# Optimization experiments

Measured on AMD Instinct MI355X. Metric: run time of the kernel, lower is better.

Reference implementation:

```python
import jax, jax.numpy as jnp
import numpy as np

N = 100000
E = 3200000
HEADS = 4
DH = 16  # per-head dim
IN = 300
OUT2 = 32
SLOPE = 0.2  # PyG GATConv leaky_relu negative slope


def setup_inputs() -> dict:
    key = jax.random.key(0)
    ks = jax.random.split(key, 10)
    x = jax.random.normal(ks[0], (N, IN), dtype=jnp.float32)
    edge_index = jax.random.randint(ks[1], (2, E), 0, N, dtype=jnp.int64)
    sec_order_edge_index = jax.random.randint(ks[2], (2, E), 0, N, dtype=jnp.int64)
    # GATConv(300, 16, heads=4) params
    W1 = jax.random.normal(ks[3], (IN, HEADS * DH), dtype=jnp.float32) * (1.0 / np.sqrt(IN))
    att_src = jax.random.normal(ks[4], (HEADS, DH), dtype=jnp.float32) * 0.1
    att_dst = jax.random.normal(ks[5], (HEADS, DH), dtype=jnp.float32) * 0.1
    b1 = jnp.zeros((HEADS * DH,), dtype=jnp.float32)
    # GCNConv(64, 32) params
    W2 = jax.random.normal(ks[6], (HEADS * DH, OUT2), dtype=jnp.float32) * (1.0 / np.sqrt(HEADS * DH))
    b2 = jnp.zeros((OUT2,), dtype=jnp.float32)
    return {"x": x, "W1": W1, "att_src": att_src, "att_dst": att_dst, "b1": b1,
            "W2": W2, "b2": b2, "edge_index": edge_index,
            "sec_order_edge_index": sec_order_edge_index}


def _add_self_loops(edge_index, n):
    loop = jnp.arange(n, dtype=edge_index.dtype)
    src = jnp.concatenate([edge_index[0], loop])
    dst = jnp.concatenate([edge_index[1], loop])
    return src, dst


def _gat(x, W1, att_src, att_dst, b1, edge_index):
    n = x.shape[0]
    src, dst = _add_self_loops(edge_index, n)
    h = (x @ W1).reshape(n, HEADS, DH)                    # [N,H,D]
    a_s = jnp.einsum('nhd,hd->nh', h, att_src)            # [N,H]
    a_d = jnp.einsum('nhd,hd->nh', h, att_dst)
    e = jax.nn.leaky_relu(a_s[src] + a_d[dst], SLOPE)     # [Et,H]
    # segment softmax over edges grouped by destination node
    m = jax.ops.segment_max(e, dst, num_segments=n)       # [N,H]
    ex = jnp.exp(e - m[dst])
    denom = jax.ops.segment_sum(ex, dst, num_segments=n)  # [N,H] (>0: self-loops)
    alpha = ex / denom[dst]                               # [Et,H]
    out = jax.ops.segment_sum(h[src] * alpha[:, :, None], dst, num_segments=n)
    return out.reshape(n, HEADS * DH) + b1


def _gcn(x, W2, b2, edge_index):
    n = x.shape[0]
    src, dst = _add_self_loops(edge_index, n)
    deg = jax.ops.segment_sum(jnp.ones_like(dst, dtype=x.dtype), dst, num_segments=n)
    dinv = jnp.where(deg > 0, jax.lax.rsqrt(deg), 0.0)
    norm = dinv[src] * dinv[dst]                          # [Et]
    h = x @ W2                                            # [N,32]
    out = jax.ops.segment_sum(h[src] * norm[:, None], dst, num_segments=n)
    return out + b2


def reference(x, W1, att_src, att_dst, b1, W2, b2, edge_index, sec_order_edge_index):
    x1 = jax.nn.relu(_gat(x, W1, att_src, att_dst, b1, edge_index))
    # F.dropout with training=False is identity (eval mode)
    return _gcn(x1, W2, b2, sec_order_edge_index)
```

## Files before the change

kernel.cpp:

```cpp
#include <hip/hip_runtime.h>
#include <hip/hip_fp16.h>

#define N_NODES 100000
#define N_EDGES 3200000
#define TOT_E   (N_EDGES + N_NODES)
#define HEADS   4
#define DH      16
#define IN_F    300
#define HID     64
#define OUT2    32
#define SLOPE   0.2f
#define NBK     256
#define GSZ     391
#define EBLK    4096
#define NBA     ((TOT_E + EBLK - 1) / EBLK)

#define G1B_ROWS 64
#define G1B_KT   20
#define G1B_NT   15
#define G1B_XP   76

__global__ __launch_bounds__(64, 2) void k_gemm1(const float* __restrict__ x,
                                                 const float* __restrict__ W1,
                                                 __half* __restrict__ h16) {
    __shared__ __align__(16) float xT[G1B_KT][G1B_XP];
    __shared__ __align__(16) float wl[2][G1B_KT * HID];
    const int t = threadIdx.x;
    const int tc = t & 7, tr = t >> 3;
    const int c0 = tc * 8, r0 = tr * 8;
    const int row0 = blockIdx.x * G1B_ROWS;

    int rj[5], qj[5];
    const float* xp[5];
#pragma unroll
    for (int j = 0; j < 5; j++) {
        int c = j * 64 + t;
        int r = c / 5;
        rj[j] = r;
        qj[j] = c - r * 5;
        int gr = row0 + r;
        gr = (gr < N_NODES) ? gr : (N_NODES - 1);
        xp[j] = x + (size_t)gr * IN_F + qj[j] * 4;
    }

    float acc[8][8];
#pragma unroll
    for (int i = 0; i < 8; i++)
#pragma unroll
        for (int j = 0; j < 8; j++) acc[i][j] = 0.f;

    float4 xr[5];
#pragma unroll
    for (int j = 0; j < 5; j++) xr[j] = *(const float4*)(xp[j]);
#pragma unroll
    for (int m = 0; m < 5; m++)
        __builtin_amdgcn_global_load_lds(
            (const __attribute__((address_space(1))) unsigned int*)(W1 + m * 256 + t * 4),
            (__attribute__((address_space(3))) unsigned int*)(&wl[0][m * 256]),
            16, 0, 0);

    for (int tt = 0; tt < G1B_NT; ++tt) {
#pragma unroll
        for (int j = 0; j < 5; j++) {
            int r = rj[j], kq = qj[j] * 4;
            xT[kq + 0][r] = xr[j].x;
            xT[kq + 1][r] = xr[j].y;
            xT[kq + 2][r] = xr[j].z;
            xT[kq + 3][r] = xr[j].w;
        }
        asm volatile("s_waitcnt vmcnt(0)" ::: "memory");
        if (tt + 1 < G1B_NT) {
            const int kt = (tt + 1) * G1B_KT;
#pragma unroll
            for (int j = 0; j < 5; j++) xr[j] = *(const float4*)(xp[j] + kt);
            const float* wsrc = W1 + kt * HID;
            float* wdst = wl[(tt + 1) & 1];
#pragma unroll
            for (int m = 0; m < 5; m++)
                __builtin_amdgcn_global_load_lds(
                    (const __attribute__((address_space(1))) unsigned int*)(wsrc + m * 256 + t * 4),
                    (__attribute__((address_space(3))) unsigned int*)(wdst + m * 256),
                    16, 0, 0);
        }
        const float* wb = wl[tt & 1];
#pragma unroll 4
        for (int k = 0; k < G1B_KT; k++) {
            float4 xa = *(const float4*)&xT[k][r0];
            float4 xb = *(const float4*)&xT[k][r0 + 4];
            float4 wa = *(const float4*)&wb[k * HID + c0];
            float4 wc = *(const float4*)&wb[k * HID + c0 + 4];
            float xv[8] = {xa.x, xa.y, xa.z, xa.w, xb.x, xb.y, xb.z, xb.w};
            float wv[8] = {wa.x, wa.y, wa.z, wa.w, wc.x, wc.y, wc.z, wc.w};
#pragma unroll
            for (int i = 0; i < 8; i++)
#pragma unroll
                for (int j = 0; j < 8; j++)
                    acc[i][j] += xv[i] * wv[j];
        }
    }

#pragma unroll
    for (int i = 0; i < 8; i++) {
        int gr = row0 + r0 + i;
        if (gr < N_NODES) {
            __half2 q[4];
            q[0] = __floats2half2_rn(acc[i][0], acc[i][1]);
            q[1] = __floats2half2_rn(acc[i][2], acc[i][3]);
            q[2] = __floats2half2_rn(acc[i][4], acc[i][5]);
            q[3] = __floats2half2_rn(acc[i][6], acc[i][7]);
            *(float4*)&h16[(size_t)gr * HID + c0] = *(float4*)q;
        }
    }
}

__global__ void k_scores(const __half* __restrict__ h16,
                         const float* __restrict__ att_src,
                         const float* __restrict__ att_dst,
                         float* __restrict__ as_ad) {
    int tid = blockIdx.x * blockDim.x + threadIdx.x;
    if (tid >= N_NODES * HEADS) return;
    int n = tid >> 2, hd = tid & 3;
    const __half* hp = &h16[(size_t)n * HID + hd * DH];
    __half2 hv[8];
    *(float4*)&hv[0] = *(const float4*)hp;
    *(float4*)&hv[4] = *(const float4*)(hp + 8);
    float s = 0.f, d = 0.f;
#pragma unroll
    for (int k = 0; k < 8; k++) {
        float2 f = __half22float2(hv[k]);
        s += f.x * att_src[hd * DH + 2 * k] + f.y * att_src[hd * DH + 2 * k + 1];
        d += f.x * att_dst[hd * DH + 2 * k] + f.y * att_dst[hd * DH + 2 * k + 1];
    }
    as_ad[n * 8 + hd] = s;
    as_ad[n * 8 + 4 + hd] = d;
}

__global__ __launch_bounds__(512) void k_chist(const int* __restrict__ ei1,
                                               const int* __restrict__ ei2,
                                               int* __restrict__ ccnt) {
    __shared__ int hist[NBK];
    int b = blockIdx.x; const int* ei; int* cc;
    if (b < NBA) { ei = ei1; cc = ccnt; }
    else         { ei = ei2; cc = ccnt + NBK; b -= NBA; }
    int t = threadIdx.x;
    if (t < NBK) hist[t] = 0;
    __syncthreads();
    int e0 = b * EBLK;
#pragma unroll
    for (int i = 0; i < 8; i++) {
        int e = e0 + i * 512 + t;
        if (e < TOT_E) {
            int dst = (e < N_EDGES) ? ei[N_EDGES + e] : (e - N_EDGES);
            atomicAdd(&hist[(unsigned int)dst / GSZ], 1);
        }
    }
    __syncthreads();
    if (t < NBK) { int v = hist[t]; if (v) atomicAdd(&cc[t], v); }
}

__global__ __launch_bounds__(512) void k_cscan(const int* __restrict__ ccnt,
                                               int* __restrict__ crp,
                                               int* __restrict__ ccur) {
    __shared__ int sc[512];
    int t = threadIdx.x;
    int idx = t & (NBK - 1);
    int own = ccnt[t];
    sc[t] = own;
    __syncthreads();
    for (int off = 1; off < NBK; off <<= 1) {
        int v = (idx >= off) ? sc[t - off] : 0;
        __syncthreads();
        sc[t] += v;
        __syncthreads();
    }
    int ex = sc[t] - own;
    crp[t] = ex; ccur[t] = ex;
}

__global__ __launch_bounds__(512) void k_binA(const int* __restrict__ ei1,
                                              const int* __restrict__ ei2,
                                              int* __restrict__ ccur,
                                              unsigned int* __restrict__ tmp) {
    __shared__ int hist[NBK];
    __shared__ int base[NBK];
    int b = blockIdx.x; const int* ei; int loff;
    if (b < NBA) { ei = ei1; loff = 0; }
    else         { ei = ei2; loff = 1; b -= NBA; }
    int t = threadIdx.x;
    if (t < NBK) hist[t] = 0;
    __syncthreads();
    unsigned int pk[8]; int cb[8], rk[8];
    int e0 = b * EBLK;
#pragma unroll
    for (int i = 0; i < 8; i++) {
        int e = e0 + i * 512 + t;
        cb[i] = -1;
        if (e < TOT_E) {
            int src, dst;
            if (e < N_EDGES) { src = ei[e]; dst = ei[N_EDGES + e]; }
            else             { src = e - N_EDGES; dst = src; }
            unsigned int c   = (unsigned int)dst / GSZ;
            unsigned int dlo = (unsigned int)dst - c * GSZ;
            cb[i] = (int)c;
            pk[i] = (dlo << 17) | (unsigned int)src;
            rk[i] = atomicAdd(&hist[c], 1);
        }
    }
    __syncthreads();
    if (t < NBK) {
        int v = hist[t];
        base[t] = v ? atomicAdd(&ccur[loff * NBK + t], v) : 0;
    }
    __syncthreads();
    unsigned int* tp = tmp + (size_t)loff * TOT_E;
#pragma unroll
    for (int i = 0; i < 8; i++)
        if (cb[i] >= 0) tp[base[cb[i]] + rk[i]] = pk[i];
}

__global__ __launch_bounds__(256) void k_binB(const unsigned int* __restrict__ tmp,
                                              const int* __restrict__ crp,
                                              int* __restrict__ rowptr,
                                              int* __restrict__ srcs,
                                              float* __restrict__ dinv) {
    __shared__ int cnt[GSZ + 1];
    __shared__ int sc[512];
    __shared__ int cur[GSZ + 1];
    int blk = blockIdx.x;
    int l = blk >> 8, b = blk & 255;
    int t = threadIdx.x;
    int nbeg = b * GSZ;
    int ncnt = min(GSZ, N_NODES - nbeg);
    const int* crpl = crp + l * NBK;
    int ebeg = crpl[b];
    int eend = (b < NBK - 1) ? crpl[b + 1] : TOT_E;
    const unsigned int* tp = tmp + (size_t)l * TOT_E;
    for (int i = t; i < GSZ + 1; i += 256) cnt[i] = 0;
    __syncthreads();
    for (int e = ebeg + t; e < eend; e += 256)
        atomicAdd(&cnt[tp[e] >> 17], 1);
    __syncthreads();
    int t2 = t + 256;
    sc[t]  = (t  < ncnt) ? cnt[t]  : 0;
    sc[t2] = (t2 < ncnt) ? cnt[t2] : 0;
    __syncthreads();
    for (int off = 1; off < 512; off <<= 1) {
        int v0 = (t  >= off) ? sc[t  - off] : 0;
        int v1 = (t2 >= off) ? sc[t2 - off] : 0;
        __syncthreads();
        sc[t] += v0; sc[t2] += v1;
        __syncthreads();
    }
    for (int i = t; i < ncnt; i += 256) {
        int c = cnt[i];
        int gpos = ebeg + sc[i] - c;
        rowptr[l * N_NODES + nbeg + i] = gpos;
        cur[i] = gpos;
        if (l == 1) dinv[nbeg + i] = rsqrtf((float)c);
    }
    __syncthreads();
    int* so = srcs + (size_t)l * TOT_E;
    for (int e = ebeg + t; e < eend; e += 256) {
        unsigned int p = tp[e];
        int pos = atomicAdd(&cur[p >> 17], 1);
        so[pos] = (int)(p & 0x1FFFF);
    }
}

__global__ __launch_bounds__(256) void k_gat(const __half* __restrict__ h16,
                                             const float* __restrict__ as_ad,
                                             const int* __restrict__ rowptr,
                                             const int* __restrict__ srcs,
                                             const float* __restrict__ b1,
                                             float* __restrict__ x1) {
    int w = (blockIdx.x * 256 + threadIdx.x) >> 6;
    if (w >= N_NODES) return;
    int lane = threadIdx.x & 63;
    int eidx = lane >> 3;
    int cl = lane & 7;
    int hd = cl >> 1;
    int c0 = cl * 8;
    float ad = as_ad[w * 8 + 4 + hd];
    int beg = rowptr[w];
    int end = (w == N_NODES - 1) ? TOT_E : rowptr[w + 1];
    float l = 0.f;
    float a0 = 0.f, a1 = 0.f, a2 = 0.f, a3 = 0.f;
    float a4 = 0.f, a5 = 0.f, a6 = 0.f, a7 = 0.f;
#pragma unroll 2
    for (int j = beg; j < end; j += 8) {
        int je = j + eidx;
        int s = srcs[min(je, end - 1)];
        float4 raw = *(const float4*)&h16[(size_t)s * HID + c0];
        float e = as_ad[s * 8 + hd] + ad;
        e = fminf(fmaxf(e, SLOPE * e), 60.f);
        float p = (je < end) ? __expf(e) : 0.f;
        l += p;
        const __half2* hv = (const __half2*)&raw;
        float2 f0 = __half22float2(hv[0]);
        float2 f1 = __half22float2(hv[1]);
        float2 f2 = __half22float2(hv[2]);
        float2 f3 = __half22float2(hv[3]);
        a0 += p * f0.x; a1 += p * f0.y; a2 += p * f1.x; a3 += p * f1.y;
        a4 += p * f2.x; a5 += p * f2.y; a6 += p * f3.x; a7 += p * f3.y;
    }
    l  += __shfl_xor(l, 8, 64);  l  += __shfl_xor(l, 16, 64);  l  += __shfl_xor(l, 32, 64);
    a0 += __shfl_xor(a0, 8, 64); a0 += __shfl_xor(a0, 16, 64); a0 += __shfl_xor(a0, 32, 64);
    a1 += __shfl_xor(a1, 8, 64); a1 += __shfl_xor(a1, 16, 64); a1 += __shfl_xor(a1, 32, 64);
    a2 += __shfl_xor(a2, 8, 64); a2 += __shfl_xor(a2, 16, 64); a2 += __shfl_xor(a2, 32, 64);
    a3 += __shfl_xor(a3, 8, 64); a3 += __shfl_xor(a3, 16, 64); a3 += __shfl_xor(a3, 32, 64);
    a4 += __shfl_xor(a4, 8, 64); a4 += __shfl_xor(a4, 16, 64); a4 += __shfl_xor(a4, 32, 64);
    a5 += __shfl_xor(a5, 8, 64); a5 += __shfl_xor(a5, 16, 64); a5 += __shfl_xor(a5, 32, 64);
    a6 += __shfl_xor(a6, 8, 64); a6 += __shfl_xor(a6, 16, 64); a6 += __shfl_xor(a6, 32, 64);
    a7 += __shfl_xor(a7, 8, 64); a7 += __shfl_xor(a7, 16, 64); a7 += __shfl_xor(a7, 32, 64);
    if (eidx == 0) {
        float rl = 1.f / l;
        float4 b0 = *(const float4*)&b1[c0];
        float4 b4 = *(const float4*)&b1[c0 + 4];
        float4 o0 = make_float4(fmaxf(a0 * rl + b0.x, 0.f),
                                fmaxf(a1 * rl + b0.y, 0.f),
                                fmaxf(a2 * rl + b0.z, 0.f),
                                fmaxf(a3 * rl + b0.w, 0.f));
        float4 o4 = make_float4(fmaxf(a4 * rl + b4.x, 0.f),
                                fmaxf(a5 * rl + b4.y, 0.f),
                                fmaxf(a6 * rl + b4.z, 0.f),
                                fmaxf(a7 * rl + b4.w, 0.f));
        *(float4*)&x1[(size_t)w * HID + c0] = o0;
        *(float4*)&x1[(size_t)w * HID + c0 + 4] = o4;
    }
}

__global__ __launch_bounds__(256) void k_gemm2(const float* __restrict__ x1,
                                               const float* __restrict__ W2,
                                               const float* __restrict__ dinv,
                                               float* __restrict__ h2s) {
    __shared__ float wl[HID * OUT2];
    __shared__ float xl[8][HID];
    int t = threadIdx.x;
    for (int i = t; i < HID * OUT2; i += 256) wl[i] = W2[i];
    int row0 = blockIdx.x * 8;
    for (int i = t; i < 8 * HID; i += 256) {
        int rr = i >> 6, kk = i & 63;
        int gr = row0 + rr;
        xl[rr][kk] = (gr < N_NODES) ? x1[(size_t)gr * HID + kk] : 0.f;
    }
    __syncthreads();
    int r = t >> 5, c = t & 31;
    float acc = 0.f;
#pragma unroll 8
    for (int k = 0; k < HID; k++) acc += xl[r][k] * wl[k * OUT2 + c];
    int gr = row0 + r;
    if (gr < N_NODES) h2s[(size_t)gr * OUT2 + c] = acc * dinv[gr];
}

__global__ __launch_bounds__(256) void k_gcn(const float* __restrict__ h2s,
                                             const float* __restrict__ dinv,
                                             const int* __restrict__ rowptr,
                                             const int* __restrict__ srcs,
                                             const float* __restrict__ b2,
                                             float* __restrict__ out) {
    int w = (blockIdx.x * 256 + threadIdx.x) >> 6;
    if (w >= N_NODES) return;
    int lane = threadIdx.x & 63;
    int eidx = lane >> 3;
    int cq = lane & 7;
    int c0 = cq * 4;
    int beg = rowptr[w];
    int end = (w == N_NODES - 1) ? TOT_E : rowptr[w + 1];
    float ax = 0.f, ay = 0.f, az = 0.f, aw = 0.f;
#pragma unroll 2
    for (int j = beg; j < end; j += 8) {
        int je = j + eidx;
        int s = srcs[min(je, end - 1)];
        float4 h4 = *(const float4*)&h2s[(size_t)s * OUT2 + c0];
        if (je < end) { ax += h4.x; ay += h4.y; az += h4.z; aw += h4.w; }
    }
    ax += __shfl_xor(ax, 8, 64); ax += __shfl_xor(ax, 16, 64); ax += __shfl_xor(ax, 32, 64);
    ay += __shfl_xor(ay, 8, 64); ay += __shfl_xor(ay, 16, 64); ay += __shfl_xor(ay, 32, 64);
    az += __shfl_xor(az, 8, 64); az += __shfl_xor(az, 16, 64); az += __shfl_xor(az, 32, 64);
    aw += __shfl_xor(aw, 8, 64); aw += __shfl_xor(aw, 16, 64); aw += __shfl_xor(aw, 32, 64);
    if (eidx == 0) {
        float dv = dinv[w];
        float4 bv = *(const float4*)&b2[c0];
        float4 o = make_float4(ax * dv + bv.x, ay * dv + bv.y,
                               az * dv + bv.z, aw * dv + bv.w);
        *(float4*)&out[(size_t)w * OUT2 + c0] = o;
    }
}

static inline size_t align_up(size_t v, size_t a) { return (v + a - 1) & ~(a - 1); }

extern "C" void kernel_launch(void* const* d_in, const int* in_sizes, int n_in,
                              void* d_out, int out_size, void* d_ws, size_t ws_size,
                              hipStream_t stream) {
    const float* x       = (const float*)d_in[0];
    const float* W1      = (const float*)d_in[1];
    const float* att_src = (const float*)d_in[2];
    const float* att_dst = (const float*)d_in[3];
    const float* b1      = (const float*)d_in[4];
    const float* W2      = (const float*)d_in[5];
    const float* b2      = (const float*)d_in[6];
    const int*   ei1     = (const int*)d_in[7];
    const int*   ei2     = (const int*)d_in[8];
    float* out = (float*)d_out;

    char* p = (char*)d_ws;
    size_t off = 0;
    auto carve = [&](size_t bytes) { void* q = p + off; off = align_up(off + bytes, 256); return q; };
    __half* h16   = (__half*)carve((size_t)N_NODES * HID * 2);
    float* x1     = (float*)carve((size_t)N_NODES * HID * 4);
    float* h2s    = (float*)carve((size_t)N_NODES * OUT2 * 4);
    float* as_ad  = (float*)carve((size_t)N_NODES * 8 * 4);
    float* dinv   = (float*)carve((size_t)N_NODES * 4);
    int* rowptr   = (int*)carve((size_t)2 * N_NODES * 4);
    int* srcs     = (int*)carve((size_t)2 * TOT_E * 4);
    int* ccnt     = (int*)carve((size_t)2 * NBK * 4);
    int* crp      = (int*)carve((size_t)2 * NBK * 4);
    int* ccur     = (int*)carve((size_t)2 * NBK * 4);
    unsigned int* tmp = (unsigned int*)x1;
    (void)ws_size; (void)in_sizes; (void)n_in; (void)out_size;

    hipMemsetAsync(ccnt, 0, (size_t)2 * NBK * 4, stream);

    k_gemm1<<<(N_NODES + G1B_ROWS - 1) / G1B_ROWS, 64, 0, stream>>>(x, W1, h16);
    k_scores<<<(N_NODES * HEADS + 255) / 256, 256, 0, stream>>>(h16, att_src, att_dst, as_ad);

    k_chist<<<2 * NBA, 512, 0, stream>>>(ei1, ei2, ccnt);
    k_cscan<<<1, 512, 0, stream>>>(ccnt, crp, ccur);
    k_binA<<<2 * NBA, 512, 0, stream>>>(ei1, ei2, ccur, tmp);
    k_binB<<<2 * NBK, 256, 0, stream>>>(tmp, crp, rowptr, srcs, dinv);

    k_gat<<<N_NODES / 4, 256, 0, stream>>>(h16, as_ad, rowptr, srcs, b1, x1);

    k_gemm2<<<N_NODES / 8, 256, 0, stream>>>(x1, W2, dinv, h2s);

    k_gcn<<<N_NODES / 4, 256, 0, stream>>>(h2s, dinv, rowptr + N_NODES, srcs + TOT_E, b2, out);
}
```

Baseline: 572.2 us.

## Use fp16 MFMA for first GEMM and store GCN features in half precision

Replaces the scalar fp32 FMA GEMM for x@W1 with an MFMA 16x16x32 f16 kernel. x is converted to fp16 into swizzled LDS tiles, and a small pre-kernel writes W1 transposed and padded as fp16. Separately, the GCN pre-aggregation features h2s are stored as fp16, which halves the bytes read per edge in the gather, and the gcn kernel now handles 16 edges per iteration with 8 channels per lane. Both changes trade precision for lower compute and memory traffic, and add one extra small kernel launch.

```diff
diff --git a/kernel.cpp b/kernel.cpp
--- a/kernel.cpp
+++ b/kernel.cpp
@@ -15,100 +15,138 @@
 #define EBLK    4096
 #define NBA     ((TOT_E + EBLK - 1) / EBLK)
 
-#define G1B_ROWS 64
-#define G1B_KT   20
-#define G1B_NT   15
-#define G1B_XP   76
-
-__global__ __launch_bounds__(64, 2) void k_gemm1(const float* __restrict__ x,
-                                                 const float* __restrict__ W1,
-                                                 __half* __restrict__ h16) {
-    __shared__ __align__(16) float xT[G1B_KT][G1B_XP];
-    __shared__ __align__(16) float wl[2][G1B_KT * HID];
+typedef _Float16 f16x8 __attribute__((ext_vector_type(8)));
+typedef float    f32x4 __attribute__((ext_vector_type(4)));
+
+__global__ void k_wcvt(const float* __restrict__ W1, __half* __restrict__ BT16) {
+    int idx = blockIdx.x * 256 + threadIdx.x;
+    if (idx >= HID * 320) return;
+    int n = idx / 320, k = idx - n * 320;
+    BT16[idx] = (k < IN_F) ? __float2half(W1[(size_t)k * HID + n]) : __float2half(0.f);
+}
+
+#define G1_BM 128
+#define G1_BK 64
+#define G1_NS 5
+
+__global__ __launch_bounds__(256) void k_gemm1(const float* __restrict__ x,
+                                               const __half* __restrict__ BT16,
+                                               __half* __restrict__ h16) {
+    __shared__ _Float16 At[G1_BM][G1_BK];
+    __shared__ _Float16 Bt[HID][G1_BK];
     const int t = threadIdx.x;
-    const int tc = t & 7, tr = t >> 3;
-    const int c0 = tc * 8, r0 = tr * 8;
-    const int row0 = blockIdx.x * G1B_ROWS;
-
-    int rj[5], qj[5];
-    const float* xp[5];
-#pragma unroll
-    for (int j = 0; j < 5; j++) {
-        int c = j * 64 + t;
-        int r = c / 5;
-        rj[j] = r;
-        qj[j] = c - r * 5;
-        int gr = row0 + r;
+    const int lane = t & 63, w = t >> 6;
+    const int lr = lane & 15, lg = lane >> 4;
+    const int row0 = blockIdx.x * G1_BM;
+    const int wrow = w * 32;
+
+    int arow[4], auc[4];
+    const float* axp[4];
+#pragma unroll
+    for (int m = 0; m < 4; m++) {
+        int id = t + m * 256;
+        arow[m] = id >> 3; auc[m] = id & 7;
+        int gr = row0 + arow[m];
         gr = (gr < N_NODES) ? gr : (N_NODES - 1);
-        xp[j] = x + (size_t)gr * IN_F + qj[j] * 4;
-    }
-
-    float acc[8][8];
-#pragma unroll
-    for (int i = 0; i < 8; i++)
-#pragma unroll
-        for (int j = 0; j < 8; j++) acc[i][j] = 0.f;
-
-    float4 xr[5];
-#pragma unroll
-    for (int j = 0; j < 5; j++) xr[j] = *(const float4*)(xp[j]);
-#pragma unroll
-    for (int m = 0; m < 5; m++)
-        __builtin_amdgcn_global_load_lds(
-            (const __attribute__((address_space(1))) unsigned int*)(W1 + m * 256 + t * 4),
-            (__attribute__((address_space(3))) unsigned int*)(&wl[0][m * 256]),
-            16, 0, 0);
-
-    for (int tt = 0; tt < G1B_NT; ++tt) {
-#pragma unroll
-        for (int j = 0; j < 5; j++) {
-            int r = rj[j], kq = qj[j] * 4;
-            xT[kq + 0][r] = xr[j].x;
-            xT[kq + 1][r] = xr[j].y;
-            xT[kq + 2][r] = xr[j].z;
-            xT[kq + 3][r] = xr[j].w;
-        }
-        asm volatile("s_waitcnt vmcnt(0)" ::: "memory");
-        if (tt + 1 < G1B_NT) {
-            const int kt = (tt + 1) * G1B_KT;
-#pragma unroll
-            for (int j = 0; j < 5; j++) xr[j] = *(const float4*)(xp[j] + kt);
-            const float* wsrc = W1 + kt * HID;
-            float* wdst = wl[(tt + 1) & 1];
-#pragma unroll
-            for (int m = 0; m < 5; m++)
-                __builtin_amdgcn_global_load_lds(
-                    (const __attribute__((address_space(1))) unsigned int*)(wsrc + m * 256 + t * 4),
-                    (__attribute__((address_space(3))) unsigned int*)(wdst + m * 256),
-                    16, 0, 0);
-        }
-        const float* wb = wl[tt & 1];
-#pragma unroll 4
-        for (int k = 0; k < G1B_KT; k++) {
-            float4 xa = *(const float4*)&xT[k][r0];
-            float4 xb = *(const float4*)&xT[k][r0 + 4];
-            float4 wa = *(const float4*)&wb[k * HID + c0];
-            float4 wc = *(const float4*)&wb[k * HID + c0 + 4];
-            float xv[8] = {xa.x, xa.y, xa.z, xa.w, xb.x, xb.y, xb.z, xb.w};
-            float wv[8] = {wa.x, wa.y, wa.z, wa.w, wc.x, wc.y, wc.z, wc.w};
-#pragma unroll
-            for (int i = 0; i < 8; i++)
-#pragma unroll
-                for (int j = 0; j < 8; j++)
-                    acc[i][j] += xv[i] * wv[j];
-        }
-    }
-
-#pragma unroll
-    for (int i = 0; i < 8; i++) {
-        int gr = row0 + r0 + i;
-        if (gr < N_NODES) {
-            __half2 q[4];
-            q[0] = __floats2half2_rn(acc[i][0], acc[i][1]);
-            q[1] = __floats2half2_rn(acc[i][2], acc[i][3]);
-            q[2] = __floats2half2_rn(acc[i][4], acc[i][5]);
-            q[3] = __floats2half2_rn(acc[i][6], acc[i][7]);
-            *(float4*)&h16[(size_t)gr * HID + c0] = *(float4*)q;
+        axp[m] = x + (size_t)gr * IN_F + auc[m] * 8;
+    }
+    int bn[2], buc[2];
+    const __half* bxp[2];
+#pragma unroll
+    for (int q = 0; q < 2; q++) {
+        int id = t + q * 256;
+        bn[q] = id >> 3; buc[q] = id & 7;
+        bxp[q] = BT16 + bn[q] * (G1_BK * G1_NS) + buc[q] * 8;
+    }
+
+    float4 ar[4][2];
+    uint4  br[2];
+
+    auto loadS = [&](int kb) {
+        if (kb + G1_BK <= IN_F) {
+#pragma unroll
+            for (int m = 0; m < 4; m++) {
+                ar[m][0] = *(const float4*)(axp[m] + kb);
+                ar[m][1] = *(const float4*)(axp[m] + kb + 4);
+            }
+        } else {
+#pragma unroll
+            for (int m = 0; m < 4; m++) {
+                float v[8];
+#pragma unroll
+                for (int e = 0; e < 8; e++) {
+                    int k = kb + auc[m] * 8 + e;
+                    v[e] = (k < IN_F) ? axp[m][kb + e] : 0.f;
+                }
+                ar[m][0] = make_float4(v[0], v[1], v[2], v[3]);
+                ar[m][1] = make_float4(v[4], v[5], v[6], v[7]);
+            }
+        }
+#pragma unroll
+        for (int q = 0; q < 2; q++) br[q] = *(const uint4*)(bxp[q] + kb);
+    };
+
+    auto writeS = [&]() {
+#pragma unroll
+        for (int m = 0; m < 4; m++) {
+            f16x8 pk;
+            pk[0] = (_Float16)ar[m][0].x; pk[1] = (_Float16)ar[m][0].y;
+            pk[2] = (_Float16)ar[m][0].z; pk[3] = (_Float16)ar[m][0].w;
+            pk[4] = (_Float16)ar[m][1].x; pk[5] = (_Float16)ar[m][1].y;
+            pk[6] = (_Float16)ar[m][1].z; pk[7] = (_Float16)ar[m][1].w;
+            *(f16x8*)&At[arow[m]][(auc[m] ^ (arow[m] & 7)) << 3] = pk;
+        }
+#pragma unroll
+        for (int q = 0; q < 2; q++)
+            *(uint4*)&Bt[bn[q]][(buc[q] ^ (bn[q] & 7)) << 3] = br[q];
+    };
+
+    f32x4 acc[2][4];
+#pragma unroll
+    for (int mt = 0; mt < 2; mt++)
+#pragma unroll
+        for (int nt = 0; nt < 4; nt++) acc[mt][nt] = (f32x4){0.f, 0.f, 0.f, 0.f};
+
+    loadS(0);
+    for (int s = 0; s < G1_NS; s++) {
+        __syncthreads();
+        writeS();
+        if (s + 1 < G1_NS) loadS((s + 1) * G1_BK);
+        __syncthreads();
+#pragma unroll
+        for (int ks = 0; ks < 2; ks++) {
+            const int u = ks * 4 + lg;
+            f16x8 af[2], bf[4];
+#pragma unroll
+            for (int mt = 0; mt < 2; mt++) {
+                int r = wrow + mt * 16 + lr;
+                af[mt] = *(const f16x8*)&At[r][(u ^ (r & 7)) << 3];
+            }
+#pragma unroll
+            for (int nt = 0; nt < 4; nt++) {
+                int n = nt * 16 + lr;
+                bf[nt] = *(const f16x8*)&Bt[n][(u ^ (n & 7)) << 3];
+            }
+#pragma unroll
+            for (int mt = 0; mt < 2; mt++)
+#pragma unroll
+                for (int nt = 0; nt < 4; nt++)
+                    acc[mt][nt] = __builtin_amdgcn_mfma_f32_16x16x32_f16(
+                        af[mt], bf[nt], acc[mt][nt], 0, 0, 0);
+        }
+    }
+
+#pragma unroll
+    for (int mt = 0; mt < 2; mt++) {
+#pragma unroll
+        for (int rg = 0; rg < 4; rg++) {
+            int gr = row0 + wrow + mt * 16 + lg * 4 + rg;
+            if (gr < N_NODES) {
+#pragma unroll
+                for (int nt = 0; nt < 4; nt++)
+                    h16[(size_t)gr * HID + nt * 16 + lr] =
+                        __float2half((float)acc[mt][nt][rg]);
+            }
         }
     }
 }
@@ -332,7 +370,7 @@
 __global__ __launch_bounds__(256) void k_gemm2(const float* __restrict__ x1,
                                                const float* __restrict__ W2,
                                                const float* __restrict__ dinv,
-                                               float* __restrict__ h2s) {
+                                               __half* __restrict__ h2s) {
     __shared__ float wl[HID * OUT2];
     __shared__ float xl[8][HID];
     int t = threadIdx.x;
@@ -349,10 +387,10 @@
 #pragma unroll 8
     for (int k = 0; k < HID; k++) acc += xl[r][k] * wl[k * OUT2 + c];
     int gr = row0 + r;
-    if (gr < N_NODES) h2s[(size_t)gr * OUT2 + c] = acc * dinv[gr];
-}
-
-__global__ __launch_bounds__(256) void k_gcn(const float* __restrict__ h2s,
+    if (gr < N_NODES) h2s[(size_t)gr * OUT2 + c] = __float2half(acc * dinv[gr]);
+}
+
+__global__ __launch_bounds__(256) void k_gcn(const __half* __restrict__ h2s,
                                              const float* __restrict__ dinv,
                                              const int* __restrict__ rowptr,
                                              const int* __restrict__ srcs,
@@ -361,29 +399,46 @@
     int w = (blockIdx.x * 256 + threadIdx.x) >> 6;
     if (w >= N_NODES) return;
     int lane = threadIdx.x & 63;
-    int eidx = lane >> 3;
-    int cq = lane & 7;
-    int c0 = cq * 4;
+    int eidx = lane >> 2;
+    int cq = lane & 3;
+    int c0 = cq * 8;
     int beg = rowptr[w];
     int end = (w == N_NODES - 1) ? TOT_E : rowptr[w + 1];
-    float ax = 0.f, ay = 0.f, az = 0.f, aw = 0.f;
+    float a0 = 0.f, a1 = 0.f, a2 = 0.f, a3 = 0.f;
+    float a4 = 0.f, a5 = 0.f, a6 = 0.f, a7 = 0.f;
 #pragma unroll 2
-    for (int j = beg; j < end; j += 8) {
+    for (int j = beg; j < end; j += 16) {
         int je = j + eidx;
         int s = srcs[min(je, end - 1)];
-        float4 h4 = *(const float4*)&h2s[(size_t)s * OUT2 + c0];
-        if (je < end) { ax += h4.x; ay += h4.y; az += h4.z; aw += h4.w; }
-    }
-    ax += __shfl_xor(ax, 8, 64); ax += __shfl_xor(ax, 16, 64); ax += __shfl_xor(ax, 32, 64);
-    ay += __shfl_xor(ay, 8, 64); ay += __shfl_xor(ay, 16, 64); ay += __shfl_xor(ay, 32, 64);
-    az += __shfl_xor(az, 8, 64); az += __shfl_xor(az, 16, 64); az += __shfl_xor(az, 32, 64);
-    aw += __shfl_xor(aw, 8, 64); aw += __shfl_xor(aw, 16, 64); aw += __shfl_xor(aw, 32, 64);
+        uint4 raw = *(const uint4*)&h2s[(size_t)s * OUT2 + c0];
+        if (je < end) {
+            const __half2* hv = (const __half2*)&raw;
+            float2 f0 = __half22float2(hv[0]);
+            float2 f1 = __half22float2(hv[1]);
+            float2 f2 = __half22float2(hv[2]);
+            float2 f3 = __half22float2(hv[3]);
+            a0 += f0.x; a1 += f0.y; a2 += f1.x; a3 += f1.y;
+            a4 += f2.x; a5 += f2.y; a6 += f3.x; a7 += f3.y;
+        }
+    }
+    a0 += __shfl_xor(a0, 4, 64); a0 += __shfl_xor(a0, 8, 64); a0 += __shfl_xor(a0, 16, 64); a0 += __shfl_xor(a0, 32, 64);
+    a1 += __shfl_xor(a1, 4, 64); a1 += __shfl_xor(a1, 8, 64); a1 += __shfl_xor(a1, 16, 64); a1 += __shfl_xor(a1, 32, 64);
+    a2 += __shfl_xor(a2, 4, 64); a2 += __shfl_xor(a2, 8, 64); a2 += __shfl_xor(a2, 16, 64); a2 += __shfl_xor(a2, 32, 64);
+    a3 += __shfl_xor(a3, 4, 64); a3 += __shfl_xor(a3, 8, 64); a3 += __shfl_xor(a3, 16, 64); a3 += __shfl_xor(a3, 32, 64);
+    a4 += __shfl_xor(a4, 4, 64); a4 += __shfl_xor(a4, 8, 64); a4 += __shfl_xor(a4, 16, 64); a4 += __shfl_xor(a4, 32, 64);
+    a5 += __shfl_xor(a5, 4, 64); a5 += __shfl_xor(a5, 8, 64); a5 += __shfl_xor(a5, 16, 64); a5 += __shfl_xor(a5, 32, 64);
+    a6 += __shfl_xor(a6, 4, 64); a6 += __shfl_xor(a6, 8, 64); a6 += __shfl_xor(a6, 16, 64); a6 += __shfl_xor(a6, 32, 64);
+    a7 += __shfl_xor(a7, 4, 64); a7 += __shfl_xor(a7, 8, 64); a7 += __shfl_xor(a7, 16, 64); a7 += __shfl_xor(a7, 32, 64);
     if (eidx == 0) {
         float dv = dinv[w];
-        float4 bv = *(const float4*)&b2[c0];
-        float4 o = make_float4(ax * dv + bv.x, ay * dv + bv.y,
-                               az * dv + bv.z, aw * dv + bv.w);
-        *(float4*)&out[(size_t)w * OUT2 + c0] = o;
+        float4 b0 = *(const float4*)&b2[c0];
+        float4 b4 = *(const float4*)&b2[c0 + 4];
+        float4 o0 = make_float4(a0 * dv + b0.x, a1 * dv + b0.y,
+                                a2 * dv + b0.z, a3 * dv + b0.w);
+        float4 o4 = make_float4(a4 * dv + b4.x, a5 * dv + b4.y,
+                                a6 * dv + b4.z, a7 * dv + b4.w);
+        *(float4*)&out[(size_t)w * OUT2 + c0] = o0;
+        *(float4*)&out[(size_t)w * OUT2 + c0 + 4] = o4;
     }
 }
 
@@ -408,7 +463,7 @@
     auto carve = [&](size_t bytes) { void* q = p + off; off = align_up(off + bytes, 256); return q; };
     __half* h16   = (__half*)carve((size_t)N_NODES * HID * 2);
     float* x1     = (float*)carve((size_t)N_NODES * HID * 4);
-    float* h2s    = (float*)carve((size_t)N_NODES * OUT2 * 4);
+    __half* h2s   = (__half*)carve((size_t)N_NODES * OUT2 * 2);
     float* as_ad  = (float*)carve((size_t)N_NODES * 8 * 4);
     float* dinv   = (float*)carve((size_t)N_NODES * 4);
     int* rowptr   = (int*)carve((size_t)2 * N_NODES * 4);
@@ -416,12 +471,14 @@
     int* ccnt     = (int*)carve((size_t)2 * NBK * 4);
     int* crp      = (int*)carve((size_t)2 * NBK * 4);
     int* ccur     = (int*)carve((size_t)2 * NBK * 4);
+    __half* BT16  = (__half*)carve((size_t)HID * 320 * 2);
     unsigned int* tmp = (unsigned int*)x1;
     (void)ws_size; (void)in_sizes; (void)n_in; (void)out_size;
 
     hipMemsetAsync(ccnt, 0, (size_t)2 * NBK * 4, stream);
 
-    k_gemm1<<<(N_NODES + G1B_ROWS - 1) / G1B_ROWS, 64, 0, stream>>>(x, W1, h16);
+    k_wcvt<<<(HID * 320 + 255) / 256, 256, 0, stream>>>(W1, BT16);
+    k_gemm1<<<(N_NODES + G1_BM - 1) / G1_BM, 256, 0, stream>>>(x, BT16, h16);
     k_scores<<<(N_NODES * HEADS + 255) / 256, 256, 0, stream>>>(h16, att_src, att_dst, as_ad);
 
     k_chist<<<2 * NBA, 512, 0, stream>>>(ei1, ei2, ccnt);
```

New measurement: 553.9 us. 3.2% less time.
